# Optimization experiments

Hardware: AMD Instinct MI355X
Metric: run time of the kernel (lower is better)

Reference implementation:

```python
import jax, jax.numpy as jnp
import numpy as np

B, T, D, L = 64, 512, 1024, 32


def setup_inputs() -> dict:
    key = jax.random.key(0)
    ks = jax.random.split(key, 6)
    x = jax.random.normal(ks[0], (B, T, D), jnp.float32)
    W = jax.random.normal(ks[1], (D, L), jnp.float32) * 0.02  # TruncatedNormal(stddev=0.02) analogue
    b = jnp.zeros((L,), jnp.float32)
    transitions = jax.random.normal(ks[2], (L, L), jnp.float32) * 0.1
    label = jax.random.randint(ks[3], (B, T), 0, L).astype(jnp.int32)
    seqlen = jax.random.randint(ks[4], (B,), 1, T + 1).astype(jnp.int32)
    mask = jnp.arange(T)[None, :] < seqlen[:, None]
    return {"x": x, "W": W, "b": b, "transitions": transitions,
            "label": label, "seqlen": seqlen, "mask": mask}


def crf_sequence_score(emissions, label, seqlen, transitions):
    # emissions: [B,T,L]
    Bc, Tc, Lc = emissions.shape
    m = (jnp.arange(Tc)[None, :] < seqlen[:, None]).astype(emissions.dtype)  # [B,T]
    unary = jnp.take_along_axis(emissions, label[..., None].astype(jnp.int32), axis=-1)[..., 0]
    unary = jnp.sum(unary * m, axis=1)
    trans = transitions[label[:, :-1], label[:, 1:]]  # [B,T-1]
    mt = (jnp.arange(1, Tc)[None, :] < seqlen[:, None]).astype(emissions.dtype)
    binary = jnp.sum(trans * mt, axis=1)
    return unary + binary


def crf_log_norm(emissions, seqlen, transitions):
    Bc, Tc, Lc = emissions.shape
    alpha0 = emissions[:, 0]  # [B,L]
    valid = (jnp.arange(1, Tc)[None, :] < seqlen[:, None]).T  # [T-1,B]
    emits = jnp.moveaxis(emissions[:, 1:], 1, 0)  # [T-1,B,L]

    def step(alpha, inp):
        emit_t, v = inp
        new = jax.nn.logsumexp(alpha[:, :, None] + transitions[None], axis=1) + emit_t
        return jnp.where(v[:, None], new, alpha), None

    alpha, _ = jax.lax.scan(step, alpha0, (emits, valid))
    return jax.nn.logsumexp(alpha, axis=-1)  # [B]


def crf_decode(emissions, transitions, seqlen):
    Bc, Tc, Lc = emissions.shape
    alpha0 = emissions[:, 0]
    idx = jnp.arange(Lc, dtype=jnp.int32)
    valid = (jnp.arange(1, Tc)[None, :] < seqlen[:, None]).T  # [T-1,B]
    emits = jnp.moveaxis(emissions[:, 1:], 1, 0)

    def fwd(alpha, inp):
        emit_t, v = inp
        scores = alpha[:, :, None] + transitions[None]  # [B,L,L]
        best = jnp.max(scores, axis=1) + emit_t
        bp = jnp.argmax(scores, axis=1).astype(jnp.int32)  # [B,L]
        alpha_new = jnp.where(v[:, None], best, alpha)
        bp = jnp.where(v[:, None], bp, idx[None, :])  # identity bp on padded steps
        return alpha_new, bp

    alpha, bps = jax.lax.scan(fwd, alpha0, (emits, valid))  # bps: [T-1,B,L]
    last = jnp.argmax(alpha, axis=-1).astype(jnp.int32)  # [B]

    def bwd(tag, bp):
        prev = jnp.take_along_axis(bp, tag[:, None], axis=1)[:, 0]
        return prev, tag

    first, tags = jax.lax.scan(bwd, last, bps, reverse=True)  # tags[i] = tag at t=i+1
    seq = jnp.concatenate([first[None], tags], axis=0)  # [T,B]
    return jnp.moveaxis(seq, 0, 1)  # [B,T]


def reference(x, W, b, transitions, label, seqlen, mask):
    emissions = jnp.einsum('btd,dl->btl', x, W) + b  # Dense projection
    ll = crf_sequence_score(emissions, label, seqlen, transitions) - crf_log_norm(emissions, seqlen, transitions)
    loss = jnp.mean(-ll)
    vit = crf_decode(emissions, transitions, seqlen)
    tp = jnp.sum(((label > 0) & (vit == label)).astype(jnp.float32))
    tn = jnp.sum(((label > 0) & (vit != label)).astype(jnp.float32))
    fp = jnp.sum((mask & (label == 0) & (vit > 0)).astype(jnp.float32))
    return loss, vit, tp, tn, fp
```

## Files before the change

kernel.cpp:

```cpp
#include <hip/hip_runtime.h>
#include <stdint.h>
#include <math.h>

#define Bn 64
#define Tn 512
#define Dn 1024
#define Ln 32
#define LOG2E 1.4426950408889634f
#define LN2f  0.6931471805599453f

#define EMIS_OFF 0
#define LOGNORM_OFF (Bn * Tn * Ln)
#define SCORE_OFF (LOGNORM_OFF + Bn)
#define CNT_OFF (SCORE_OFF + Bn)

#define BM 128
#define KB 32
#define XSS 132

__global__ __launch_bounds__(256) void gemm_emis(
    const float* __restrict__ x, const float* __restrict__ Wm,
    const float* __restrict__ bias, const int* __restrict__ seqlen,
    float* __restrict__ emis)
{
    int b  = blockIdx.x >> 2;
    int t0 = (blockIdx.x & 3) * BM;
    if (t0 >= seqlen[b]) return;

    __shared__ __align__(16) float xs[KB * XSS];
    __shared__ __align__(16) float wsh[KB * Ln];

    int tid = threadIdx.x;
    int cg = tid & 7;
    int rg = tid >> 3;

    const float* xrow = x + (size_t)(b * Tn + t0) * Dn;

    float acc[4][4];
    #pragma unroll
    for (int z = 0; z < 4; z++)
        #pragma unroll
        for (int c = 0; c < 4; c++) acc[z][c] = 0.f;

    float4 xr[4]; float4 wr;
    #pragma unroll
    for (int u = 0; u < 4; u++) {
        int f = tid + 256 * u;
        xr[u] = *(const float4*)(xrow + (size_t)(f >> 3) * Dn + (f & 7) * 4);
    }
    wr = *(const float4*)(Wm + tid * 4);

    for (int k0 = 0; k0 < Dn; k0 += KB) {
        __syncthreads();
        #pragma unroll
        for (int u = 0; u < 4; u++) {
            int f = tid + 256 * u;
            int lrow = f >> 3, kk = f & 7;
            xs[(4 * kk + 0) * XSS + lrow] = xr[u].x;
            xs[(4 * kk + 1) * XSS + lrow] = xr[u].y;
            xs[(4 * kk + 2) * XSS + lrow] = xr[u].z;
            xs[(4 * kk + 3) * XSS + lrow] = xr[u].w;
        }
        *(float4*)(wsh + tid * 4) = wr;
        __syncthreads();

        int kn = k0 + KB;
        if (kn < Dn) {
            #pragma unroll
            for (int u = 0; u < 4; u++) {
                int f = tid + 256 * u;
                xr[u] = *(const float4*)(xrow + (size_t)(f >> 3) * Dn + kn + (f & 7) * 4);
            }
            wr = *(const float4*)(Wm + (size_t)kn * Ln + tid * 4);
        }

        #pragma unroll 8
        for (int k = 0; k < KB; k++) {
            float4 a = *(const float4*)(xs + k * XSS + 4 * rg);
            float4 w = *(const float4*)(wsh + k * Ln + 4 * cg);
            float av[4] = {a.x, a.y, a.z, a.w};
            float wv[4] = {w.x, w.y, w.z, w.w};
            #pragma unroll
            for (int z = 0; z < 4; z++)
                #pragma unroll
                for (int c = 0; c < 4; c++)
                    acc[z][c] = fmaf(av[z], wv[c], acc[z][c]);
        }
    }

    float4 bv = *(const float4*)(bias + 4 * cg);
    float bb[4] = {bv.x, bv.y, bv.z, bv.w};
    #pragma unroll
    for (int z = 0; z < 4; z++) {
        float4 o;
        o.x = acc[z][0] + bb[0];
        o.y = acc[z][1] + bb[1];
        o.z = acc[z][2] + bb[2];
        o.w = acc[z][3] + bb[3];
        *(float4*)(emis + (size_t)(b * Tn + t0 + 4 * rg + z) * Ln + 4 * cg) = o;
    }
}

#define CH 64

__global__ __launch_bounds__(512) void crf_forward(
    const float* __restrict__ emis, const float* __restrict__ trans,
    const int* __restrict__ label, const int* __restrict__ seqlen,
    float* __restrict__ out, float* __restrict__ wsf)
{
    __shared__ __align__(16) float es[Tn * Ln];
    __shared__ __align__(16) float al[Tn * Ln];
    __shared__ __align__(16) float trs[Ln * Ln];
    __shared__ __align__(16) float abuf[Ln];
    __shared__ __align__(16) float lbuf[Ln];
    __shared__ uint8_t bp[Tn * Ln];
    __shared__ uint8_t Fm[16 * 32];
    __shared__ int btag[16];
    __shared__ int s_last;
    __shared__ float credA[8], credB[8], credC[8];

    int tid = threadIdx.x;
    int b = blockIdx.x;
    int slen = seqlen[b];
    int wv = tid >> 6;
    int lane = tid & 63;
    int j = lane & 31;

    const float* eb = emis + (size_t)b * Tn * Ln;

    {
        int n4 = slen * (Ln / 4);
        for (int i4 = tid; i4 < n4; i4 += 512)
            ((float4*)es)[i4] = ((const float4*)eb)[i4];
    }
    if (tid < 256) ((float4*)trs)[tid] = ((const float4*)trans)[tid];
    {
        uint32_t* bp32 = (uint32_t*)bp;
        for (int w = tid; w < Tn * Ln / 4; w += 512)
            bp32[w] = 0x03020100u + 0x04040404u * (uint32_t)(w & 7);
    }
    __syncthreads();

    float av = 0.f, emit = 0.f;
    float a = 0.f, eemit = 0.f;
    int   Eacc = 0;
    float tr[32];
    float e2[32];

    if (wv == 0) {
        #pragma unroll
        for (int i = 0; i < 32; i++) tr[i] = trs[i * Ln + j];
        av = es[j];
        if (lane < 32) al[j] = av;
        emit = es[Ln + j];
    } else if (wv == 1) {
        #pragma unroll
        for (int i = 0; i < 32; i++) e2[i] = exp2f(trs[i * Ln + j] * LOG2E);
        a = exp2f(es[j] * LOG2E);
        eemit = exp2f(es[Ln + j] * LOG2E);
    } else {
        #pragma unroll
        for (int i = 0; i < 32; i++) tr[i] = trs[i * Ln + j];
    }

    for (int c = 0; c < Tn / CH; c++) {
        int tb = (c == 0) ? 1 : c * CH;
        int te = (c + 1) * CH; if (te > slen) te = slen;

        if (wv == 0) {
            for (int t = tb; t < te; t++) {
                int tnx = (t + 1 < slen) ? (t + 1) : (slen - 1);
                if (lane < 32) abuf[j] = av;
                float emitn = es[tnx * Ln + j];
                float4 A0 = *(const float4*)(abuf + 0);
                float4 A1 = *(const float4*)(abuf + 4);
                float4 A2 = *(const float4*)(abuf + 8);
                float4 A3 = *(const float4*)(abuf + 12);
                float4 A4 = *(const float4*)(abuf + 16);
                float4 A5 = *(const float4*)(abuf + 20);
                float4 A6 = *(const float4*)(abuf + 24);
                float4 A7 = *(const float4*)(abuf + 28);
                float vv[32];
                vv[0]=A0.x+tr[0];   vv[1]=A0.y+tr[1];   vv[2]=A0.z+tr[2];   vv[3]=A0.w+tr[3];
                vv[4]=A1.x+tr[4];   vv[5]=A1.y+tr[5];   vv[6]=A1.z+tr[6];   vv[7]=A1.w+tr[7];
                vv[8]=A2.x+tr[8];   vv[9]=A2.y+tr[9];   vv[10]=A2.z+tr[10]; vv[11]=A2.w+tr[11];
                vv[12]=A3.x+tr[12]; vv[13]=A3.y+tr[13]; vv[14]=A3.z+tr[14]; vv[15]=A3.w+tr[15];
                vv[16]=A4.x+tr[16]; vv[17]=A4.y+tr[17]; vv[18]=A4.z+tr[18]; vv[19]=A4.w+tr[19];
                vv[20]=A5.x+tr[20]; vv[21]=A5.y+tr[21]; vv[22]=A5.z+tr[22]; vv[23]=A5.w+tr[23];
                vv[24]=A6.x+tr[24]; vv[25]=A6.y+tr[25]; vv[26]=A6.z+tr[26]; vv[27]=A6.w+tr[27];
                vv[28]=A7.x+tr[28]; vv[29]=A7.y+tr[29]; vv[30]=A7.z+tr[30]; vv[31]=A7.w+tr[31];
                float u[11];
                #pragma unroll
                for (int g = 0; g < 10; g++)
                    u[g] = fmaxf(fmaxf(vv[3*g], vv[3*g+1]), vv[3*g+2]);
                u[10] = fmaxf(vv[30], vv[31]);
                float w0 = fmaxf(fmaxf(u[0], u[1]), u[2]);
                float w1 = fmaxf(fmaxf(u[3], u[4]), u[5]);
                float w2 = fmaxf(fmaxf(u[6], u[7]), u[8]);
                float w3 = fmaxf(u[9], u[10]);
                av = fmaxf(fmaxf(w0, w1), fmaxf(w2, w3)) + emit;
                if (lane < 32) al[t * Ln + j] = av;
                emit = emitn;
            }
        } else if (wv == 1) {
            for (int t = tb; t < te; t++) {
                int tnx = (t + 1 < slen) ? (t + 1) : (slen - 1);
                if (lane < 32) lbuf[j] = a;
                float emitn = es[tnx * Ln + j];
                float4 A0 = *(const float4*)(lbuf + 0);
                float4 A1 = *(const float4*)(lbuf + 4);
                float4 A2 = *(const float4*)(lbuf + 8);
                float4 A3 = *(const float4*)(lbuf + 12);
                float4 A4 = *(const float4*)(lbuf + 16);
                float4 A5 = *(const float4*)(lbuf + 20);
                float4 A6 = *(const float4*)(lbuf + 24);
                float4 A7 = *(const float4*)(lbuf + 28);
                float eemitn = exp2f(emitn * LOG2E);
                float s0, s1, s2, s3;
                s0 = A0.x * e2[0];  s1 = A0.y * e2[1];  s2 = A0.z * e2[2];  s3 = A0.w * e2[3];
                s0 = fmaf(A1.x, e2[4], s0);  s1 = fmaf(A1.y, e2[5], s1);
                s2 = fmaf(A1.z, e2[6], s2);  s3 = fmaf(A1.w, e2[7], s3);
                s0 = fmaf(A2.x, e2[8], s0);  s1 = fmaf(A2.y, e2[9], s1);
                s2 = fmaf(A2.z, e2[10], s2); s3 = fmaf(A2.w, e2[11], s3);
                s0 = fmaf(A3.x, e2[12], s0); s1 = fmaf(A3.y, e2[13], s1);
                s2 = fmaf(A3.z, e2[14], s2); s3 = fmaf(A3.w, e2[15], s3);
                s0 = fmaf(A4.x, e2[16], s0); s1 = fmaf(A4.y, e2[17], s1);
                s2 = fmaf(A4.z, e2[18], s2); s3 = fmaf(A4.w, e2[19], s3);
                s0 = fmaf(A5.x, e2[20], s0); s1 = fmaf(A5.y, e2[21], s1);
                s2 = fmaf(A5.z, e2[22], s2); s3 = fmaf(A5.w, e2[23], s3);
                s0 = fmaf(A6.x, e2[24], s0); s1 = fmaf(A6.y, e2[25], s1);
                s2 = fmaf(A6.z, e2[26], s2); s3 = fmaf(A6.w, e2[27], s3);
                s0 = fmaf(A7.x, e2[28], s0); s1 = fmaf(A7.y, e2[29], s1);
                s2 = fmaf(A7.z, e2[30], s2); s3 = fmaf(A7.w, e2[31], s3);
                float s = ((s0 + s1) + (s2 + s3)) * eemit;
                if ((t & 3) == 0) {
                    unsigned sb = (unsigned)__builtin_amdgcn_readfirstlane(__float_as_int(s));
                    int e = (int)((sb >> 23) & 0xFFu) - 127;
                    Eacc += e;
                    a = ldexpf(s, -e);
                } else {
                    a = s;
                }
                eemit = eemitn;
            }
        } else if (c == 0) {
            if (wv == 2) {
                const int* lb = label + (size_t)b * Tn;
                float acc = 0.f;
                for (int t = lane; t < Tn; t += 64) {
                    if (t < slen) {
                        int lc = lb[t];
                        acc += es[t * Ln + lc];
                        if (t >= 1) acc += trs[lb[t - 1] * Ln + lc];
                    }
                }
                #pragma unroll
                for (int off = 32; off >= 1; off >>= 1) acc += __shfl_xor(acc, off);
                if (lane == 0) wsf[SCORE_OFF + b] = acc;
            }
        } else {
            int stripe = (wv - 2) * 2 + (lane >> 5);
            int pb = ((c - 1) == 0) ? 1 : (c - 1) * CH;
            int pe = c * CH; if (pe > slen) pe = slen;
            for (int t = pb + stripe; t < pe; t += 12) {
                const float* ar = al + (t - 1) * Ln;
                float vv[32];
                #pragma unroll
                for (int i = 0; i < 32; i += 4) {
                    float4 a4 = *(const float4*)(ar + i);
                    vv[i]     = a4.x + tr[i];
                    vv[i + 1] = a4.y + tr[i + 1];
                    vv[i + 2] = a4.z + tr[i + 2];
                    vv[i + 3] = a4.w + tr[i + 3];
                }
                float mv[16]; int mi[16];
                #pragma unroll
                for (int i = 0; i < 16; i++) {
                    bool g = vv[2*i+1] > vv[2*i];
                    mv[i] = g ? vv[2*i+1] : vv[2*i];
                    mi[i] = g ? (2*i+1) : (2*i);
                }
                #pragma unroll
                for (int i = 0; i < 8; i++) {
                    bool g = mv[2*i+1] > mv[2*i];
                    mv[i] = g ? mv[2*i+1] : mv[2*i];
                    mi[i] = g ? mi[2*i+1] : mi[2*i];
                }
                #pragma unroll
                for (int i = 0; i < 4; i++) {
                    bool g = mv[2*i+1] > mv[2*i];
                    mv[i] = g ? mv[2*i+1] : mv[2*i];
                    mi[i] = g ? mi[2*i+1] : mi[2*i];
                }
                #pragma unroll
                for (int i = 0; i < 2; i++) {
                    bool g = mv[2*i+1] > mv[2*i];
                    mv[i] = g ? mv[2*i+1] : mv[2*i];
                    mi[i] = g ? mi[2*i+1] : mi[2*i];
                }
                bp[t * Ln + j] = (uint8_t)mi[0];
            }
        }
        __syncthreads();
    }

    if (wv == 0) {
        float mm = av; int ai = j;
        #pragma unroll
        for (int off = 16; off >= 1; off >>= 1) {
            float om = __shfl_xor(mm, off);
            int   oi = __shfl_xor(ai, off);
            if (om > mm || (om == mm && oi < ai)) { mm = om; ai = oi; }
        }
        if (lane == 0) s_last = ai;
    } else if (wv == 1) {
        float ss = a;
        #pragma unroll
        for (int off = 16; off >= 1; off >>= 1) ss += __shfl_xor(ss, off);
        if (lane == 0)
            wsf[LOGNORM_OFF + b] = fmaf(log2f(ss) + (float)Eacc, LN2f, 0.f);
    } else {
        int stripe = (wv - 2) * 2 + (lane >> 5);
        int cc = Tn / CH - 1;
        int pb = cc * CH;
        int pe = Tn; if (pe > slen) pe = slen;
        for (int t = pb + stripe; t < pe; t += 12) {
            const float* ar = al + (t - 1) * Ln;
            float vv[32];
            #pragma unroll
            for (int i = 0; i < 32; i += 4) {
                float4 a4 = *(const float4*)(ar + i);
                vv[i]     = a4.x + tr[i];
                vv[i + 1] = a4.y + tr[i + 1];
                vv[i + 2] = a4.z + tr[i + 2];
                vv[i + 3] = a4.w + tr[i + 3];
            }
            float mv[16]; int mi[16];
            #pragma unroll
            for (int i = 0; i < 16; i++) {
                bool g = vv[2*i+1] > vv[2*i];
                mv[i] = g ? vv[2*i+1] : vv[2*i];
                mi[i] = g ? (2*i+1) : (2*i);
            }
            #pragma unroll
            for (int i = 0; i < 8; i++) {
                bool g = mv[2*i+1] > mv[2*i];
                mv[i] = g ? mv[2*i+1] : mv[2*i];
                mi[i] = g ? mi[2*i+1] : mi[2*i];
            }
            #pragma unroll
            for (int i = 0; i < 4; i++) {
                bool g = mv[2*i+1] > mv[2*i];
                mv[i] = g ? mv[2*i+1] : mv[2*i];
                mi[i] = g ? mi[2*i+1] : mi[2*i];
            }
            #pragma unroll
            for (int i = 0; i < 2; i++) {
                bool g = mv[2*i+1] > mv[2*i];
                mv[i] = g ? mv[2*i+1] : mv[2*i];
                mi[i] = g ? mi[2*i+1] : mi[2*i];
            }
            bp[t * Ln + j] = (uint8_t)mi[0];
        }
    }
    __syncthreads();

    int sseg = tid >> 5, ent = tid & 31;
    {
        int y = ent;
        for (int p = 32 * sseg + 31; p >= 32 * sseg; p--) y = bp[p * Ln + y];
        Fm[sseg * 32 + ent] = (uint8_t)y;
    }
    __syncthreads();
    if (tid == 0) {
        int y = s_last;
        btag[15] = y;
        for (int ss = 15; ss >= 1; ss--) { y = Fm[ss * 32 + y]; btag[ss - 1] = y; }
    }
    __syncthreads();
    int q = tid;
    int y = btag[sseg];
    for (int p = 32 * sseg + 31; p >= q + 1; p--) y = bp[p * Ln + y];
    out[1 + (size_t)b * Tn + q] = (float)y;

    int lbl = label[(size_t)b * Tn + q];
    float tpf = (lbl > 0 && y == lbl) ? 1.f : 0.f;
    float tnf = (lbl > 0 && y != lbl) ? 1.f : 0.f;
    float fpf = (q < slen && lbl == 0 && y > 0) ? 1.f : 0.f;
    #pragma unroll
    for (int off = 32; off >= 1; off >>= 1) {
        tpf += __shfl_xor(tpf, off);
        tnf += __shfl_xor(tnf, off);
        fpf += __shfl_xor(fpf, off);
    }
    if (lane == 0) { credA[wv] = tpf; credB[wv] = tnf; credC[wv] = fpf; }
    __syncthreads();
    if (tid == 0) {
        float aa = 0.f, bb2 = 0.f, cc2 = 0.f;
        #pragma unroll
        for (int w = 0; w < 8; w++) { aa += credA[w]; bb2 += credB[w]; cc2 += credC[w]; }
        wsf[CNT_OFF + b] = aa;
        wsf[CNT_OFF + Bn + b] = bb2;
        wsf[CNT_OFF + 2 * Bn + b] = cc2;
    }
}

__global__ __launch_bounds__(64) void crf_final(const float* __restrict__ wsf,
                                                float* __restrict__ out)
{
    int lane = threadIdx.x;
    float nll = wsf[LOGNORM_OFF + lane] - wsf[SCORE_OFF + lane];
    float tp = wsf[CNT_OFF + lane];
    float tn = wsf[CNT_OFF + Bn + lane];
    float fp = wsf[CNT_OFF + 2 * Bn + lane];
    #pragma unroll
    for (int off = 32; off >= 1; off >>= 1) {
        nll += __shfl_xor(nll, off);
        tp  += __shfl_xor(tp, off);
        tn  += __shfl_xor(tn, off);
        fp  += __shfl_xor(fp, off);
    }
    if (lane == 0) {
        out[0] = nll * (1.f / 64.f);
        out[1 + Bn * Tn + 0] = tp;
        out[1 + Bn * Tn + 1] = tn;
        out[1 + Bn * Tn + 2] = fp;
    }
}

extern "C" void kernel_launch(void* const* d_in, const int* in_sizes, int n_in,
                              void* d_out, int out_size, void* d_ws, size_t ws_size,
                              hipStream_t stream) {
    const float* x     = (const float*)d_in[0];
    const float* W     = (const float*)d_in[1];
    const float* bias  = (const float*)d_in[2];
    const float* trans = (const float*)d_in[3];
    const int* label   = (const int*)d_in[4];
    const int* seqlen  = (const int*)d_in[5];
    float* out = (float*)d_out;
    float* wsf = (float*)d_ws;

    gemm_emis<<<dim3(Bn * (Tn / BM)), dim3(256), 0, stream>>>(x, W, bias, seqlen, wsf + EMIS_OFF);
    crf_forward<<<dim3(Bn), dim3(512), 0, stream>>>(wsf + EMIS_OFF, trans, label, seqlen, out, wsf);
    crf_final<<<dim3(1), dim3(64), 0, stream>>>(wsf, out);
}
```

Baseline: 319.0 us.

## Split CRF forward into separate scan and decode kernels across more blocks

The fused per-batch kernel, which ran the Viterbi max scan, the logsumexp scan and the backpointer computation in different waves of one 512-thread block, is split in two. A new 64-thread kernel with 2*B blocks runs the max scan and the log-normaliser scan in separate blocks, reading emissions straight from global memory and writing Viterbi alphas to a workspace. A second kernel then loads those alphas, computes all backpointers in parallel with no chunked synchronisation, and does the backtrace. This drops the per-chunk barriers and puts the two serial scans on different CUs, at the cost of an extra launch, a global round trip for the alphas, and global-latency emission loads inside the serial loop.

```diff
diff --git a/kernel.cpp b/kernel.cpp
--- a/kernel.cpp
+++ b/kernel.cpp
@@ -10,7 +10,8 @@
 #define LN2f  0.6931471805599453f
 
 #define EMIS_OFF 0
-#define LOGNORM_OFF (Bn * Tn * Ln)
+#define AL_OFF (Bn * Tn * Ln)
+#define LOGNORM_OFF (AL_OFF + Bn * Tn * Ln)
 #define SCORE_OFF (LOGNORM_OFF + Bn)
 #define CNT_OFF (SCORE_OFF + Bn)
 
@@ -101,18 +102,129 @@
     }
 }
 
-#define CH 64
-
-__global__ __launch_bounds__(512) void crf_forward(
+__global__ __launch_bounds__(64) void crf_scan(
+    const float* __restrict__ emis, const float* __restrict__ trans,
+    const int* __restrict__ seqlen, float* __restrict__ al_g,
+    float* __restrict__ wsf)
+{
+    __shared__ __align__(16) float abuf[64];
+
+    int lane = threadIdx.x;
+    int j = lane & 31;
+    int role = blockIdx.x >> 6;
+    int b = blockIdx.x & 63;
+    int slen = seqlen[b];
+    const float* eb = emis + (size_t)b * Tn * Ln;
+
+    if (role == 0) {
+        float tr[32];
+        #pragma unroll
+        for (int i = 0; i < 32; i++) tr[i] = trans[i * Ln + j];
+
+        float av = eb[j];
+        if (lane < 32) al_g[(size_t)b * Tn * Ln + j] = av;
+        float emit = eb[Ln + j];
+
+        for (int t = 1; t < slen; t++) {
+            int tn2 = (t + 1 < slen) ? (t + 1) : (slen - 1);
+            float emitn = eb[(size_t)tn2 * Ln + j];
+            abuf[lane] = av;
+            float4 A0 = *(const float4*)(abuf + 0);
+            float4 A1 = *(const float4*)(abuf + 4);
+            float4 A2 = *(const float4*)(abuf + 8);
+            float4 A3 = *(const float4*)(abuf + 12);
+            float4 A4 = *(const float4*)(abuf + 16);
+            float4 A5 = *(const float4*)(abuf + 20);
+            float4 A6 = *(const float4*)(abuf + 24);
+            float4 A7 = *(const float4*)(abuf + 28);
+            float vv[32];
+            vv[0]=A0.x+tr[0];   vv[1]=A0.y+tr[1];   vv[2]=A0.z+tr[2];   vv[3]=A0.w+tr[3];
+            vv[4]=A1.x+tr[4];   vv[5]=A1.y+tr[5];   vv[6]=A1.z+tr[6];   vv[7]=A1.w+tr[7];
+            vv[8]=A2.x+tr[8];   vv[9]=A2.y+tr[9];   vv[10]=A2.z+tr[10]; vv[11]=A2.w+tr[11];
+            vv[12]=A3.x+tr[12]; vv[13]=A3.y+tr[13]; vv[14]=A3.z+tr[14]; vv[15]=A3.w+tr[15];
+            vv[16]=A4.x+tr[16]; vv[17]=A4.y+tr[17]; vv[18]=A4.z+tr[18]; vv[19]=A4.w+tr[19];
+            vv[20]=A5.x+tr[20]; vv[21]=A5.y+tr[21]; vv[22]=A5.z+tr[22]; vv[23]=A5.w+tr[23];
+            vv[24]=A6.x+tr[24]; vv[25]=A6.y+tr[25]; vv[26]=A6.z+tr[26]; vv[27]=A6.w+tr[27];
+            vv[28]=A7.x+tr[28]; vv[29]=A7.y+tr[29]; vv[30]=A7.z+tr[30]; vv[31]=A7.w+tr[31];
+            float u[11];
+            #pragma unroll
+            for (int g = 0; g < 10; g++)
+                u[g] = fmaxf(fmaxf(vv[3*g], vv[3*g+1]), vv[3*g+2]);
+            u[10] = fmaxf(vv[30], vv[31]);
+            float w0 = fmaxf(fmaxf(u[0], u[1]), u[2]);
+            float w1 = fmaxf(fmaxf(u[3], u[4]), u[5]);
+            float w2 = fmaxf(fmaxf(u[6], u[7]), u[8]);
+            float w3 = fmaxf(u[9], u[10]);
+            av = fmaxf(fmaxf(w0, w1), fmaxf(w2, w3)) + emit;
+            if (lane < 32) al_g[((size_t)b * Tn + t) * Ln + j] = av;
+            emit = emitn;
+        }
+    } else {
+        float e2[32];
+        #pragma unroll
+        for (int i = 0; i < 32; i++) e2[i] = exp2f(trans[i * Ln + j] * LOG2E);
+
+        float a = exp2f(eb[j] * LOG2E);
+        float eemit = exp2f(eb[Ln + j] * LOG2E);
+        int Eacc = 0;
+
+        for (int t = 1; t < slen; t++) {
+            int tn2 = (t + 1 < slen) ? (t + 1) : (slen - 1);
+            float emitn = eb[(size_t)tn2 * Ln + j];
+            abuf[lane] = a;
+            float4 A0 = *(const float4*)(abuf + 0);
+            float4 A1 = *(const float4*)(abuf + 4);
+            float4 A2 = *(const float4*)(abuf + 8);
+            float4 A3 = *(const float4*)(abuf + 12);
+            float4 A4 = *(const float4*)(abuf + 16);
+            float4 A5 = *(const float4*)(abuf + 20);
+            float4 A6 = *(const float4*)(abuf + 24);
+            float4 A7 = *(const float4*)(abuf + 28);
+            float eemitn = exp2f(emitn * LOG2E);
+            float s0, s1, s2, s3;
+            s0 = A0.x * e2[0];  s1 = A0.y * e2[1];  s2 = A0.z * e2[2];  s3 = A0.w * e2[3];
+            s0 = fmaf(A1.x, e2[4], s0);  s1 = fmaf(A1.y, e2[5], s1);
+            s2 = fmaf(A1.z, e2[6], s2);  s3 = fmaf(A1.w, e2[7], s3);
+            s0 = fmaf(A2.x, e2[8], s0);  s1 = fmaf(A2.y, e2[9], s1);
+            s2 = fmaf(A2.z, e2[10], s2); s3 = fmaf(A2.w, e2[11], s3);
+            s0 = fmaf(A3.x, e2[12], s0); s1 = fmaf(A3.y, e2[13], s1);
+            s2 = fmaf(A3.z, e2[14], s2); s3 = fmaf(A3.w, e2[15], s3);
+            s0 = fmaf(A4.x, e2[16], s0); s1 = fmaf(A4.y, e2[17], s1);
+            s2 = fmaf(A4.z, e2[18], s2); s3 = fmaf(A4.w, e2[19], s3);
+            s0 = fmaf(A5.x, e2[20], s0); s1 = fmaf(A5.y, e2[21], s1);
+            s2 = fmaf(A5.z, e2[22], s2); s3 = fmaf(A5.w, e2[23], s3);
+            s0 = fmaf(A6.x, e2[24], s0); s1 = fmaf(A6.y, e2[25], s1);
+            s2 = fmaf(A6.z, e2[26], s2); s3 = fmaf(A6.w, e2[27], s3);
+            s0 = fmaf(A7.x, e2[28], s0); s1 = fmaf(A7.y, e2[29], s1);
+            s2 = fmaf(A7.z, e2[30], s2); s3 = fmaf(A7.w, e2[31], s3);
+            float s = ((s0 + s1) + (s2 + s3)) * eemit;
+            if ((t & 3) == 0) {
+                unsigned sb = (unsigned)__builtin_amdgcn_readfirstlane(__float_as_int(s));
+                int e = (int)((sb >> 23) & 0xFFu) - 127;
+                Eacc += e;
+                a = ldexpf(s, -e);
+            } else {
+                a = s;
+            }
+            eemit = eemitn;
+        }
+
+        float ss = a;
+        #pragma unroll
+        for (int off = 16; off >= 1; off >>= 1) ss += __shfl_xor(ss, off);
+        if (lane == 0)
+            wsf[LOGNORM_OFF + b] = fmaf(log2f(ss) + (float)Eacc, LN2f, 0.f);
+    }
+}
+
+__global__ __launch_bounds__(512) void crf_decode(
     const float* __restrict__ emis, const float* __restrict__ trans,
     const int* __restrict__ label, const int* __restrict__ seqlen,
-    float* __restrict__ out, float* __restrict__ wsf)
+    const float* __restrict__ al_g, float* __restrict__ out,
+    float* __restrict__ wsf)
 {
-    __shared__ __align__(16) float es[Tn * Ln];
-    __shared__ __align__(16) float al[Tn * Ln];
+    __shared__ __align__(16) float al_s[Tn * Ln];
     __shared__ __align__(16) float trs[Ln * Ln];
-    __shared__ __align__(16) float abuf[Ln];
-    __shared__ __align__(16) float lbuf[Ln];
     __shared__ uint8_t bp[Tn * Ln];
     __shared__ uint8_t Fm[16 * 32];
     __shared__ int btag[16];
@@ -126,12 +238,11 @@
     int lane = tid & 63;
     int j = lane & 31;
 
-    const float* eb = emis + (size_t)b * Tn * Ln;
-
     {
+        const float4* src = (const float4*)(al_g + (size_t)b * Tn * Ln);
         int n4 = slen * (Ln / 4);
         for (int i4 = tid; i4 < n4; i4 += 512)
-            ((float4*)es)[i4] = ((const float4*)eb)[i4];
+            ((float4*)al_s)[i4] = src[i4];
     }
     if (tid < 256) ((float4*)trs)[tid] = ((const float4*)trans)[tid];
     {
@@ -141,171 +252,23 @@
     }
     __syncthreads();
 
-    float av = 0.f, emit = 0.f;
-    float a = 0.f, eemit = 0.f;
-    int   Eacc = 0;
-    float tr[32];
-    float e2[32];
-
     if (wv == 0) {
-        #pragma unroll
-        for (int i = 0; i < 32; i++) tr[i] = trs[i * Ln + j];
-        av = es[j];
-        if (lane < 32) al[j] = av;
-        emit = es[Ln + j];
-    } else if (wv == 1) {
-        #pragma unroll
-        for (int i = 0; i < 32; i++) e2[i] = exp2f(trs[i * Ln + j] * LOG2E);
-        a = exp2f(es[j] * LOG2E);
-        eemit = exp2f(es[Ln + j] * LOG2E);
-    } else {
-        #pragma unroll
-        for (int i = 0; i < 32; i++) tr[i] = trs[i * Ln + j];
-    }
-
-    for (int c = 0; c < Tn / CH; c++) {
-        int tb = (c == 0) ? 1 : c * CH;
-        int te = (c + 1) * CH; if (te > slen) te = slen;
-
-        if (wv == 0) {
-            for (int t = tb; t < te; t++) {
-                int tnx = (t + 1 < slen) ? (t + 1) : (slen - 1);
-                if (lane < 32) abuf[j] = av;
-                float emitn = es[tnx * Ln + j];
-                float4 A0 = *(const float4*)(abuf + 0);
-                float4 A1 = *(const float4*)(abuf + 4);
-                float4 A2 = *(const float4*)(abuf + 8);
-                float4 A3 = *(const float4*)(abuf + 12);
-                float4 A4 = *(const float4*)(abuf + 16);
-                float4 A5 = *(const float4*)(abuf + 20);
-                float4 A6 = *(const float4*)(abuf + 24);
-                float4 A7 = *(const float4*)(abuf + 28);
-                float vv[32];
-                vv[0]=A0.x+tr[0];   vv[1]=A0.y+tr[1];   vv[2]=A0.z+tr[2];   vv[3]=A0.w+tr[3];
-                vv[4]=A1.x+tr[4];   vv[5]=A1.y+tr[5];   vv[6]=A1.z+tr[6];   vv[7]=A1.w+tr[7];
-                vv[8]=A2.x+tr[8];   vv[9]=A2.y+tr[9];   vv[10]=A2.z+tr[10]; vv[11]=A2.w+tr[11];
-                vv[12]=A3.x+tr[12]; vv[13]=A3.y+tr[13]; vv[14]=A3.z+tr[14]; vv[15]=A3.w+tr[15];
-                vv[16]=A4.x+tr[16]; vv[17]=A4.y+tr[17]; vv[18]=A4.z+tr[18]; vv[19]=A4.w+tr[19];
-                vv[20]=A5.x+tr[20]; vv[21]=A5.y+tr[21]; vv[22]=A5.z+tr[22]; vv[23]=A5.w+tr[23];
-                vv[24]=A6.x+tr[24]; vv[25]=A6.y+tr[25]; vv[26]=A6.z+tr[26]; vv[27]=A6.w+tr[27];
-                vv[28]=A7.x+tr[28]; vv[29]=A7.y+tr[29]; vv[30]=A7.z+tr[30]; vv[31]=A7.w+tr[31];
-                float u[11];
-                #pragma unroll
-                for (int g = 0; g < 10; g++)
-                    u[g] = fmaxf(fmaxf(vv[3*g], vv[3*g+1]), vv[3*g+2]);
-                u[10] = fmaxf(vv[30], vv[31]);
-                float w0 = fmaxf(fmaxf(u[0], u[1]), u[2]);
-                float w1 = fmaxf(fmaxf(u[3], u[4]), u[5]);
-                float w2 = fmaxf(fmaxf(u[6], u[7]), u[8]);
-                float w3 = fmaxf(u[9], u[10]);
-                av = fmaxf(fmaxf(w0, w1), fmaxf(w2, w3)) + emit;
-                if (lane < 32) al[t * Ln + j] = av;
-                emit = emitn;
-            }
-        } else if (wv == 1) {
-            for (int t = tb; t < te; t++) {
-                int tnx = (t + 1 < slen) ? (t + 1) : (slen - 1);
-                if (lane < 32) lbuf[j] = a;
-                float emitn = es[tnx * Ln + j];
-                float4 A0 = *(const float4*)(lbuf + 0);
-                float4 A1 = *(const float4*)(lbuf + 4);
-                float4 A2 = *(const float4*)(lbuf + 8);
-                float4 A3 = *(const float4*)(lbuf + 12);
-                float4 A4 = *(const float4*)(lbuf + 16);
-                float4 A5 = *(const float4*)(lbuf + 20);
-                float4 A6 = *(const float4*)(lbuf + 24);
-                float4 A7 = *(const float4*)(lbuf + 28);
-                float eemitn = exp2f(emitn * LOG2E);
-                float s0, s1, s2, s3;
-                s0 = A0.x * e2[0];  s1 = A0.y * e2[1];  s2 = A0.z * e2[2];  s3 = A0.w * e2[3];
-                s0 = fmaf(A1.x, e2[4], s0);  s1 = fmaf(A1.y, e2[5], s1);
-                s2 = fmaf(A1.z, e2[6], s2);  s3 = fmaf(A1.w, e2[7], s3);
-                s0 = fmaf(A2.x, e2[8], s0);  s1 = fmaf(A2.y, e2[9], s1);
-                s2 = fmaf(A2.z, e2[10], s2); s3 = fmaf(A2.w, e2[11], s3);
-                s0 = fmaf(A3.x, e2[12], s0); s1 = fmaf(A3.y, e2[13], s1);
-                s2 = fmaf(A3.z, e2[14], s2); s3 = fmaf(A3.w, e2[15], s3);
-                s0 = fmaf(A4.x, e2[16], s0); s1 = fmaf(A4.y, e2[17], s1);
-                s2 = fmaf(A4.z, e2[18], s2); s3 = fmaf(A4.w, e2[19], s3);
-                s0 = fmaf(A5.x, e2[20], s0); s1 = fmaf(A5.y, e2[21], s1);
-                s2 = fmaf(A5.z, e2[22], s2); s3 = fmaf(A5.w, e2[23], s3);
-                s0 = fmaf(A6.x, e2[24], s0); s1 = fmaf(A6.y, e2[25], s1);
-                s2 = fmaf(A6.z, e2[26], s2); s3 = fmaf(A6.w, e2[27], s3);
-                s0 = fmaf(A7.x, e2[28], s0); s1 = fmaf(A7.y, e2[29], s1);
-                s2 = fmaf(A7.z, e2[30], s2); s3 = fmaf(A7.w, e2[31], s3);
-                float s = ((s0 + s1) + (s2 + s3)) * eemit;
-                if ((t & 3) == 0) {
-                    unsigned sb = (unsigned)__builtin_amdgcn_readfirstlane(__float_as_int(s));
-                    int e = (int)((sb >> 23) & 0xFFu) - 127;
-                    Eacc += e;
-                    a = ldexpf(s, -e);
-                } else {
-                    a = s;
-                }
-                eemit = eemitn;
-            }
-        } else if (c == 0) {
-            if (wv == 2) {
-                const int* lb = label + (size_t)b * Tn;
-                float acc = 0.f;
-                for (int t = lane; t < Tn; t += 64) {
-                    if (t < slen) {
-                        int lc = lb[t];
-                        acc += es[t * Ln + lc];
-                        if (t >= 1) acc += trs[lb[t - 1] * Ln + lc];
-                    }
-                }
-                #pragma unroll
-                for (int off = 32; off >= 1; off >>= 1) acc += __shfl_xor(acc, off);
-                if (lane == 0) wsf[SCORE_OFF + b] = acc;
-            }
-        } else {
-            int stripe = (wv - 2) * 2 + (lane >> 5);
-            int pb = ((c - 1) == 0) ? 1 : (c - 1) * CH;
-            int pe = c * CH; if (pe > slen) pe = slen;
-            for (int t = pb + stripe; t < pe; t += 12) {
-                const float* ar = al + (t - 1) * Ln;
-                float vv[32];
-                #pragma unroll
-                for (int i = 0; i < 32; i += 4) {
-                    float4 a4 = *(const float4*)(ar + i);
-                    vv[i]     = a4.x + tr[i];
-                    vv[i + 1] = a4.y + tr[i + 1];
-                    vv[i + 2] = a4.z + tr[i + 2];
-                    vv[i + 3] = a4.w + tr[i + 3];
-                }
-                float mv[16]; int mi[16];
-                #pragma unroll
-                for (int i = 0; i < 16; i++) {
-                    bool g = vv[2*i+1] > vv[2*i];
-                    mv[i] = g ? vv[2*i+1] : vv[2*i];
-                    mi[i] = g ? (2*i+1) : (2*i);
-                }
-                #pragma unroll
-                for (int i = 0; i < 8; i++) {
-                    bool g = mv[2*i+1] > mv[2*i];
-                    mv[i] = g ? mv[2*i+1] : mv[2*i];
-                    mi[i] = g ? mi[2*i+1] : mi[2*i];
-                }
-                #pragma unroll
-                for (int i = 0; i < 4; i++) {
-                    bool g = mv[2*i+1] > mv[2*i];
-                    mv[i] = g ? mv[2*i+1] : mv[2*i];
-                    mi[i] = g ? mi[2*i+1] : mi[2*i];
-                }
-                #pragma unroll
-                for (int i = 0; i < 2; i++) {
-                    bool g = mv[2*i+1] > mv[2*i];
-                    mv[i] = g ? mv[2*i+1] : mv[2*i];
-                    mi[i] = g ? mi[2*i+1] : mi[2*i];
-                }
-                bp[t * Ln + j] = (uint8_t)mi[0];
-            }
-        }
-        __syncthreads();
-    }
-
-    if (wv == 0) {
-        float mm = av; int ai = j;
+        const int* lb = label + (size_t)b * Tn;
+        const float* eg = emis + (size_t)b * Tn * Ln;
+        float acc = 0.f;
+        for (int t = lane; t < Tn; t += 64) {
+            if (t < slen) {
+                int lc = lb[t];
+                acc += eg[(size_t)t * Ln + lc];
+                if (t >= 1) acc += trs[lb[t - 1] * Ln + lc];
+            }
+        }
+        #pragma unroll
+        for (int off = 32; off >= 1; off >>= 1) acc += __shfl_xor(acc, off);
+        if (lane == 0) wsf[SCORE_OFF + b] = acc;
+
+        float mm = al_s[(slen - 1) * Ln + j];
+        int ai = j;
         #pragma unroll
         for (int off = 16; off >= 1; off >>= 1) {
             float om = __shfl_xor(mm, off);
@@ -313,19 +276,13 @@
             if (om > mm || (om == mm && oi < ai)) { mm = om; ai = oi; }
         }
         if (lane == 0) s_last = ai;
-    } else if (wv == 1) {
-        float ss = a;
-        #pragma unroll
-        for (int off = 16; off >= 1; off >>= 1) ss += __shfl_xor(ss, off);
-        if (lane == 0)
-            wsf[LOGNORM_OFF + b] = fmaf(log2f(ss) + (float)Eacc, LN2f, 0.f);
     } else {
-        int stripe = (wv - 2) * 2 + (lane >> 5);
-        int cc = Tn / CH - 1;
-        int pb = cc * CH;
-        int pe = Tn; if (pe > slen) pe = slen;
-        for (int t = pb + stripe; t < pe; t += 12) {
-            const float* ar = al + (t - 1) * Ln;
+        float tr[32];
+        #pragma unroll
+        for (int i = 0; i < 32; i++) tr[i] = trs[i * Ln + j];
+        int stripe = (wv - 1) * 2 + (lane >> 5);
+        for (int t = 1 + stripe; t < slen; t += 14) {
+            const float* ar = al_s + (t - 1) * Ln;
             float vv[32];
             #pragma unroll
             for (int i = 0; i < 32; i += 4) {
@@ -441,6 +398,7 @@
     float* wsf = (float*)d_ws;
 
     gemm_emis<<<dim3(Bn * (Tn / BM)), dim3(256), 0, stream>>>(x, W, bias, seqlen, wsf + EMIS_OFF);
-    crf_forward<<<dim3(Bn), dim3(512), 0, stream>>>(wsf + EMIS_OFF, trans, label, seqlen, out, wsf);
+    crf_scan<<<dim3(2 * Bn), dim3(64), 0, stream>>>(wsf + EMIS_OFF, trans, seqlen, wsf + AL_OFF, wsf);
+    crf_decode<<<dim3(Bn), dim3(512), 0, stream>>>(wsf + EMIS_OFF, trans, label, seqlen, wsf + AL_OFF, out, wsf);
     crf_final<<<dim3(1), dim3(64), 0, stream>>>(wsf, out);
 }
```

New measurement: 394.4 us. 1.24x slower.
